# Performance work log

Measured on AMD Instinct MI355X. Metric: run time of the kernel, lower is better.

## Reference

```python
import jax, jax.numpy as jnp
import numpy as np
from jax import lax

B, N, IN_DIM, OUT_DIM = 4, 8192, 32, 128
NPOINT, RADIUS, NSAMPLE = 1024, 0.2, 32
BN_EPS = 1e-5

def _sqdist(a, b):
    # a: [B,n,3], b: [B,m,3] -> [B,n,m] squared euclidean distances
    return (jnp.sum(a * a, -1)[:, :, None] + jnp.sum(b * b, -1)[:, None, :]
            - 2.0 * jnp.einsum('bnd,bmd->bnm', a, b))

def _fps(xyz, npoint):
    # farthest point sampling, sequential by nature -> lax.scan over npoint steps
    Bn, Np, _ = xyz.shape
    def step(carry, _):
        dist, far = carry
        centroid = jnp.take_along_axis(xyz, far[:, None, None], axis=1)  # [B,1,3]
        dist = jnp.minimum(dist, jnp.sum((xyz - centroid) ** 2, -1))
        return (dist, jnp.argmax(dist, -1).astype(jnp.int32)), far
    init = (jnp.full((Bn, Np), 1e10, xyz.dtype), jnp.zeros((Bn,), jnp.int32))
    _, idx = lax.scan(step, init, None, length=npoint)
    return idx.T  # [B, npoint]

def _gather_points(x, idx):  # x [B,N,D], idx [B,...] -> [B,...,D]
    return jax.vmap(lambda p, i: p[i])(x, idx)

def _gather_feats(f, idx):  # f [B,C,N], idx [B,...] -> [B,C,...]
    return jax.vmap(lambda p, i: p[:, i])(f, idx)

def _ball_query(new_xyz, xyz):
    d2 = _sqdist(new_xyz, xyz)  # [B,P,N]
    Np = xyz.shape[1]
    cand = jnp.where(d2 < RADIUS ** 2, jnp.arange(Np, dtype=jnp.int32), Np)
    idx = -lax.top_k(-cand, NSAMPLE)[0]  # first NSAMPLE in-radius indices (sorted)
    return jnp.where(idx == Np, idx[..., :1], idx)  # pad misses with first hit

def _bn(x, gamma, beta, axes):
    # training-mode batch norm over `axes`, channel axis = 1
    m = jnp.mean(x, axes, keepdims=True)
    v = jnp.var(x, axes, keepdims=True)
    sh = (1, -1) + (1,) * (x.ndim - 2)
    return (x - m) * (gamma.reshape(sh) / jnp.sqrt(v + BN_EPS)) + beta.reshape(sh)

def _forward(xyz, features, W_sa0, g_sa0, b_sa0, W_sa1, g_sa1, b_sa1, W_sa2, g_sa2, b_sa2,
             W_fp0, g_fp0, b_fp0, W_fp1, g_fp1, b_fp1,
             Wc1, bc1, g1, b1, Wc2, bc2, g2, b2, Wc3, bc3):
    # --- PointnetSAModuleVotes: FPS + ball query + group (use_xyz, normalize_xyz) + MLP + maxpool ---
    fps_idx = _fps(xyz, NPOINT)
    new_xyz = _gather_points(xyz, fps_idx)                           # [B,P,3]
    gidx = _ball_query(new_xyz, xyz)                                 # [B,P,S]
    gxyz = (_gather_points(xyz, gidx) - new_xyz[:, :, None, :]) / RADIUS  # centered, normalized
    h = jnp.concatenate([gxyz.transpose(0, 3, 1, 2), _gather_feats(features, gidx)], 1)  # [B,3+C,P,S]
    for W, g, b in ((W_sa0, g_sa0, b_sa0), (W_sa1, g_sa1, b_sa1), (W_sa2, g_sa2, b_sa2)):
        h = jax.nn.relu(_bn(jnp.einsum('oc,bcps->bops', W, h), g, b, (0, 2, 3)))
    feat_sa = jnp.max(h, -1)                                         # [B,128,P]
    # --- PointnetFPModule: 3-NN interpolation (inv-sq-dist weights) + skip concat + MLP ---
    d2 = _sqdist(xyz, new_xyz)                                       # [B,N,P]
    neg, idx3 = lax.top_k(-d2, 3)
    recip = 1.0 / (jnp.maximum(-neg, 0.0) + 1e-8)
    w = recip / jnp.sum(recip, -1, keepdims=True)                    # [B,N,3]
    interp = jnp.sum(_gather_feats(feat_sa, idx3) * w[:, None, :, :], -1)  # [B,128,N]
    h = jnp.concatenate([interp, features], 1)                       # [B,128+C,N]
    for W, g, b in ((W_fp0, g_fp0, b_fp0), (W_fp1, g_fp1, b_fp1)):
        h = jax.nn.relu(_bn(jnp.einsum('oc,bcn->bon', W, h), g, b, (0, 2)))
    seed_features = h                                                # [B,128,N]
    # --- vote head: conv1d(1) + BN + ReLU x2, then conv1d(1) -> [3 offset | 1 score | out_dim feat] ---
    net = jax.nn.relu(_bn(jnp.einsum('oc,bcn->bon', Wc1, seed_features) + bc1[:, None], g1, b1, (0, 2)))
    net = jax.nn.relu(_bn(jnp.einsum('oc,bcn->bon', Wc2, net) + bc2[:, None], g2, b2, (0, 2)))
    net = (jnp.einsum('oc,bcn->bon', Wc3, net) + bc3[:, None]).transpose(0, 2, 1)  # [B,N,4+out]
    offset = net[:, :, 0:3]
    vote_xyz = xyz + offset
    vote_scores = jax.nn.sigmoid(net[:, :, 3])
    vf = seed_features.transpose(0, 2, 1) + net[:, :, 4:]
    vote_features = vf / jnp.maximum(jnp.linalg.norm(vf, axis=2, keepdims=True), 1e-12)  # F.normalize
    return vote_xyz, offset, vote_scores, vote_features

def setup_inputs():
    key = jax.random.key(0)
    ks = jax.random.split(key, 40)
    he = lambda k, o, c: jax.random.normal(k, (o, c), jnp.float32) * float(np.sqrt(2.0 / c))
    inp = {'xyz': jax.random.uniform(ks[0], (B, N, 3), jnp.float32),
           'features': jax.random.normal(ks[1], (B, IN_DIM, N), jnp.float32)}
    j = 2
    dims_sa = [IN_DIM + 3, 128, 128, 128]  # use_xyz adds 3 to first layer
    for i in range(3):
        inp[f'W_sa{i}'] = he(ks[j], 128, dims_sa[i]); j += 1
        inp[f'g_sa{i}'] = 1.0 + 0.1 * jax.random.normal(ks[j], (128,), jnp.float32); j += 1
        inp[f'b_sa{i}'] = 0.1 * jax.random.normal(ks[j], (128,), jnp.float32); j += 1
    dims_fp = [IN_DIM + 128, 128, 128]
    for i in range(2):
        inp[f'W_fp{i}'] = he(ks[j], 128, dims_fp[i]); j += 1
        inp[f'g_fp{i}'] = 1.0 + 0.1 * jax.random.normal(ks[j], (128,), jnp.float32); j += 1
        inp[f'b_fp{i}'] = 0.1 * jax.random.normal(ks[j], (128,), jnp.float32); j += 1
    inp['Wc1'] = he(ks[j], 128, 128); j += 1
    inp['bc1'] = 0.01 * jax.random.normal(ks[j], (128,), jnp.float32); j += 1
    inp['g1'] = 1.0 + 0.1 * jax.random.normal(ks[j], (128,), jnp.float32); j += 1
    inp['b1'] = 0.1 * jax.random.normal(ks[j], (128,), jnp.float32); j += 1
    inp['Wc2'] = he(ks[j], 128, 128); j += 1
    inp['bc2'] = 0.01 * jax.random.normal(ks[j], (128,), jnp.float32); j += 1
    inp['g2'] = 1.0 + 0.1 * jax.random.normal(ks[j], (128,), jnp.float32); j += 1
    inp['b2'] = 0.1 * jax.random.normal(ks[j], (128,), jnp.float32); j += 1
    inp['Wc3'] = he(ks[j], 4 + OUT_DIM, 128); j += 1
    inp['bc3'] = 0.01 * jax.random.normal(ks[j], (4 + OUT_DIM,), jnp.float32); j += 1
    return inp

def reference(xyz, features, W_sa0, g_sa0, b_sa0, W_sa1, g_sa1, b_sa1, W_sa2, g_sa2, b_sa2,
              W_fp0, g_fp0, b_fp0, W_fp1, g_fp1, b_fp1,
              Wc1, bc1, g1, b1, Wc2, bc2, g2, b2, Wc3, bc3):
    return _forward(xyz, features, W_sa0, g_sa0, b_sa0, W_sa1, g_sa1, b_sa1, W_sa2, g_sa2, b_sa2,
                    W_fp0, g_fp0, b_fp0, W_fp1, g_fp1, b_fp1,
                    Wc1, bc1, g1, b1, Wc2, bc2, g2, b2, Wc3, bc3)
```

## Files before the change

kernel.cpp:

```cpp
#include <hip/hip_runtime.h>
#include <hip/hip_bf16.h>
#include <math.h>

namespace {

constexpr int BB  = 4;
constexpr int NN  = 8192;
constexpr int IND = 32;
constexpr int NPT = 1024;
constexpr int NSM = 32;
constexpr int SACOLS = BB * NPT * NSM;
constexpr int FPCOLS = BB * NN;
constexpr int CSTR = 132;

__device__ __forceinline__ double sqn3_f64(float x, float y, float z) {
#pragma clang fp contract(off)
    double dx = (double)x, dy = (double)y, dz = (double)z;
    return (dx * dx + dy * dy) + dz * dz;
}
__device__ __forceinline__ double dot3_f64(float ax, float ay, float az,
                                           float bx, float by, float bz) {
#pragma clang fp contract(off)
    return ((double)ax * (double)bx + (double)ay * (double)by) + (double)az * (double)bz;
}
__device__ __forceinline__ double sqd_f64(double sa, double sb, double dot) {
#pragma clang fp contract(off)
    return (sa + sb) - 2.0 * dot;
}

__global__ __launch_bounds__(512)
void k_fps(const float* __restrict__ xyz, float* __restrict__ new_xyz)
{
#pragma clang fp contract(off)
    const int b   = blockIdx.x;
    const int tid = threadIdx.x;
    const float* P = xyz + (size_t)b * NN * 3;

    __shared__ float sx[NN];
    __shared__ float sy[NN];
    __shared__ float sz[NN];
    __shared__ float ctrs[NPT * 3];
    __shared__ unsigned long long wv[2][8];

    float px[16], py[16], pz[16], dd[16];
#pragma unroll
    for (int i = 0; i < 16; ++i) {
        int p = tid + i * 512;
        float x = P[p * 3 + 0], y = P[p * 3 + 1], z = P[p * 3 + 2];
        px[i] = x; py[i] = y; pz[i] = z; dd[i] = 1e10f;
        sx[p] = x; sy[p] = y; sz[p] = z;
    }
    float cx = P[0], cy = P[1], cz = P[2];
    __syncthreads();

    for (int t = 0; t < NPT; ++t) {
        if (tid == 0) {
            ctrs[t * 3 + 0] = cx;
            ctrs[t * 3 + 1] = cy;
            ctrs[t * 3 + 2] = cz;
        }
        if (t == NPT - 1) break;

        unsigned long long best = 0ull;
#pragma unroll
        for (int i = 0; i < 16; ++i) {
            float dx = px[i] - cx;
            float dy = py[i] - cy;
            float dz = pz[i] - cz;
            float d  = (dx * dx + dy * dy) + dz * dz;
            float nd = fminf(dd[i], d);
            dd[i] = nd;
            unsigned int lo = (unsigned)(NN - 1) - (unsigned)(tid + i * 512);
            unsigned long long cand =
                ((unsigned long long)__float_as_uint(nd) << 32) | lo;
            best = (cand > best) ? cand : best;
        }
        for (int off = 32; off > 0; off >>= 1) {
            unsigned long long o = __shfl_down(best, off);
            best = (o > best) ? o : best;
        }
        const int buf = t & 1;
        if ((tid & 63) == 0) wv[buf][tid >> 6] = best;
        __syncthreads();
        unsigned long long w0 = wv[buf][0];
#pragma unroll
        for (int k = 1; k < 8; ++k) {
            unsigned long long wk = wv[buf][k];
            w0 = (wk > w0) ? wk : w0;
        }
        const int idx = (NN - 1) - (int)(unsigned)(w0 & 0xFFFFFFFFull);
        cx = sx[idx]; cy = sy[idx]; cz = sz[idx];
    }

    __syncthreads();
    float* O = new_xyz + (size_t)b * NPT * 3;
    for (int i = tid; i < NPT * 3; i += 512) O[i] = ctrs[i];
}

__global__ __launch_bounds__(256)
void k_ballquery(const float* __restrict__ xyz, const float* __restrict__ new_xyz,
                 int* __restrict__ gidx)
{
    const int wv   = threadIdx.x >> 6;
    const int lane = threadIdx.x & 63;
    const int cid  = blockIdx.x * 4 + wv;
    const int b    = cid >> 10;
    const float* P = xyz + (size_t)b * NN * 3;

    const float cx = new_xyz[(size_t)cid * 3 + 0];
    const float cy = new_xyz[(size_t)cid * 3 + 1];
    const float cz = new_xyz[(size_t)cid * 3 + 2];
    const double sa = sqn3_f64(cx, cy, cz);
    const double R2 = 0.2 * 0.2;

    int cnt = 0;
    int firstidx = -1;
    int* G = gidx + (size_t)cid * NSM;

    for (int base = 0; base < NN && cnt < NSM; base += 64) {
        int p = base + lane;
        float x = P[p * 3 + 0], y = P[p * 3 + 1], z = P[p * 3 + 2];
        double sb  = sqn3_f64(x, y, z);
        double dot = dot3_f64(cx, cy, cz, x, y, z);
        double d2  = sqd_f64(sa, sb, dot);
        bool hit = d2 < R2;
        unsigned long long m = __ballot(hit);
        if (firstidx < 0 && m != 0ull) firstidx = base + __builtin_ctzll(m);
        int before = __popcll(m & ((1ull << lane) - 1ull));
        int pos = cnt + before;
        if (hit && pos < NSM) G[pos] = p;
        cnt += __popcll(m);
    }
    if (firstidx < 0) firstidx = 0;
    if (cnt < NSM) {
        for (int j = cnt + lane; j < NSM; j += 64) G[j] = firstidx;
    }
}

__global__ __launch_bounds__(256)
void k_group(const float* __restrict__ xyz, const float* __restrict__ feats,
             const float* __restrict__ new_xyz, const int* __restrict__ gidx,
             float* __restrict__ h0)
{
    const int col = blockIdx.x * 256 + threadIdx.x;
    const int cid = col >> 5;
    const int b   = col >> 15;
    const int g   = gidx[col];
    const float* Pt = xyz + ((size_t)b * NN + g) * 3;
    const float* Ct = new_xyz + (size_t)cid * 3;
    h0[(size_t)0 * SACOLS + col] = __fsub_rn(Pt[0], Ct[0]) / 0.2f;
    h0[(size_t)1 * SACOLS + col] = __fsub_rn(Pt[1], Ct[1]) / 0.2f;
    h0[(size_t)2 * SACOLS + col] = __fsub_rn(Pt[2], Ct[2]) / 0.2f;
    const float* FT = feats + (size_t)b * IND * NN;
    for (int c = 0; c < IND; ++c)
        h0[(size_t)(3 + c) * SACOLS + col] = FT[(size_t)c * NN + g];
}

__global__ __launch_bounds__(256)
void k_conv(const float* __restrict__ X, const float* __restrict__ W,
            const float* __restrict__ bias,
            const float* __restrict__ scale, const float* __restrict__ shift,
            float* __restrict__ Z, int Cin, int Cout, int ncol, int apply_act)
{
    __shared__ __align__(16) float Xs[32][64];
    __shared__ float Ws[64][33];
    const int tid  = threadIdx.x;
    const int col0 = blockIdx.x * 64;
    const int o0   = blockIdx.y * 64;
    const int tx   = tid & 15;
    const int ty   = tid >> 4;
    float acc[4][4] = {};

    for (int kk = 0; kk < Cin; kk += 32) {
#pragma unroll
        for (int i = 0; i < 8; ++i) {
            int idx = tid + i * 256;
            int c = idx >> 6, cc = idx & 63;
            int ch = kk + c;
            float v = 0.0f;
            if (ch < Cin) {
                v = X[(size_t)ch * ncol + col0 + cc];
                if (apply_act) v = fmaxf(fmaf(v, scale[ch], shift[ch]), 0.0f);
            }
            Xs[c][cc] = v;
        }
#pragma unroll
        for (int i = 0; i < 8; ++i) {
            int idx = tid + i * 256;
            int o = idx >> 5, c = idx & 31;
            int ch = kk + c, oo = o0 + o;
            Ws[o][c] = (ch < Cin && oo < Cout) ? W[(size_t)oo * Cin + ch] : 0.0f;
        }
        __syncthreads();
#pragma unroll
        for (int c = 0; c < 32; ++c) {
            const float4 xv = *reinterpret_cast<const float4*>(&Xs[c][tx * 4]);
            float w0 = Ws[ty * 4 + 0][c];
            float w1 = Ws[ty * 4 + 1][c];
            float w2 = Ws[ty * 4 + 2][c];
            float w3 = Ws[ty * 4 + 3][c];
            acc[0][0] = fmaf(w0, xv.x, acc[0][0]); acc[0][1] = fmaf(w0, xv.y, acc[0][1]);
            acc[0][2] = fmaf(w0, xv.z, acc[0][2]); acc[0][3] = fmaf(w0, xv.w, acc[0][3]);
            acc[1][0] = fmaf(w1, xv.x, acc[1][0]); acc[1][1] = fmaf(w1, xv.y, acc[1][1]);
            acc[1][2] = fmaf(w1, xv.z, acc[1][2]); acc[1][3] = fmaf(w1, xv.w, acc[1][3]);
            acc[2][0] = fmaf(w2, xv.x, acc[2][0]); acc[2][1] = fmaf(w2, xv.y, acc[2][1]);
            acc[2][2] = fmaf(w2, xv.z, acc[2][2]); acc[2][3] = fmaf(w2, xv.w, acc[2][3]);
            acc[3][0] = fmaf(w3, xv.x, acc[3][0]); acc[3][1] = fmaf(w3, xv.y, acc[3][1]);
            acc[3][2] = fmaf(w3, xv.z, acc[3][2]); acc[3][3] = fmaf(w3, xv.w, acc[3][3]);
        }
        __syncthreads();
    }
#pragma unroll
    for (int i = 0; i < 4; ++i) {
        int o = o0 + ty * 4 + i;
        if (o >= Cout) break;
        float bz = bias ? bias[o] : 0.0f;
#pragma unroll
        for (int j = 0; j < 4; ++j)
            Z[(size_t)o * ncol + col0 + tx * 4 + j] = acc[i][j] + bz;
    }
}

__global__ __launch_bounds__(256)
void k_stats_partial(const float* __restrict__ Z, double* __restrict__ part, int ncol, int nb)
{
    const int c = blockIdx.x, blk = blockIdx.y;
    const int chunk = ncol / nb;
    const float* p = Z + (size_t)c * ncol + (size_t)blk * chunk;
    double s = 0.0, q = 0.0;
    for (int j = threadIdx.x; j < chunk; j += 256) { double v = (double)p[j]; s += v; q += v * v; }
    __shared__ double ss[256];
    __shared__ double qq[256];
    ss[threadIdx.x] = s; qq[threadIdx.x] = q;
    __syncthreads();
    for (int off = 128; off > 0; off >>= 1) {
        if (threadIdx.x < off) { ss[threadIdx.x] += ss[threadIdx.x + off]; qq[threadIdx.x] += qq[threadIdx.x + off]; }
        __syncthreads();
    }
    if (threadIdx.x == 0) {
        part[(size_t)(c * nb + blk) * 2 + 0] = ss[0];
        part[(size_t)(c * nb + blk) * 2 + 1] = qq[0];
    }
}

__global__ void k_stats_final(const double* __restrict__ part,
                              const float* __restrict__ gamma, const float* __restrict__ beta,
                              float* __restrict__ sc_out, float* __restrict__ sh_out,
                              int C, int nb, double n)
{
    int c = threadIdx.x;
    if (c >= C) return;
    double s = 0.0, q = 0.0;
    for (int i = 0; i < nb; ++i) {
        s += part[(size_t)(c * nb + i) * 2 + 0];
        q += part[(size_t)(c * nb + i) * 2 + 1];
    }
    double mean = s / n;
    double var  = q / n - mean * mean;
    double scl  = (double)gamma[c] / sqrt(var + 1e-5);
    sc_out[c] = (float)scl;
    sh_out[c] = (float)((double)beta[c] - mean * scl);
}

__global__ __launch_bounds__(256)
void k_maxpool(const float* __restrict__ Z, const float* __restrict__ sc,
               const float* __restrict__ sh, float* __restrict__ feat)
{
    const int idx = blockIdx.x * 256 + threadIdx.x;
    const int bp  = idx & 4095;
    const int c   = idx >> 12;
    const float s = sc[c], h = sh[c];
    const float* p = Z + (size_t)c * SACOLS + (size_t)bp * 32;
    float m = 0.0f;
    for (int ss = 0; ss < 32; ++ss) m = fmaxf(m, fmaxf(fmaf(p[ss], s, h), 0.0f));
    feat[(size_t)c * (BB * NPT) + bp] = m;
}

__global__ __launch_bounds__(256)
void k_3nn(const float* __restrict__ xyz, const float* __restrict__ new_xyz,
           int* __restrict__ idx3, float* __restrict__ w3)
{
    const int gid = blockIdx.x * 256 + threadIdx.x;
    const int b = gid >> 13;
    __shared__ float  cxs[NPT];
    __shared__ float  cys[NPT];
    __shared__ float  czs[NPT];
    __shared__ double cns[NPT];
    const float* C = new_xyz + (size_t)b * NPT * 3;
    for (int i = threadIdx.x; i < NPT; i += 256) {
        float x = C[i * 3], y = C[i * 3 + 1], z = C[i * 3 + 2];
        cxs[i] = x; cys[i] = y; czs[i] = z; cns[i] = sqn3_f64(x, y, z);
    }
    __syncthreads();

    const float* P = xyz + (size_t)gid * 3;
    const float px = P[0], py = P[1], pz = P[2];
    const double sb = sqn3_f64(px, py, pz);
    double d0 = 1e30, d1 = 1e30, d2v = 1e30;
    int    i0 = 0, i1 = 0, i2 = 0;
    for (int m = 0; m < NPT; ++m) {
        double dot = dot3_f64(px, py, pz, cxs[m], cys[m], czs[m]);
        double d   = sqd_f64(sb, cns[m], dot);
        if (d < d0)       { d2v = d1; i2 = i1; d1 = d0; i1 = i0; d0 = d; i0 = m; }
        else if (d < d1)  { d2v = d1; i2 = i1; d1 = d;  i1 = m; }
        else if (d < d2v) { d2v = d;  i2 = m; }
    }
    {
#pragma clang fp contract(off)
        double e0 = fmax(d0, 0.0), e1 = fmax(d1, 0.0), e2 = fmax(d2v, 0.0);
        double r0 = 1.0 / (e0 + 1e-8);
        double r1 = 1.0 / (e1 + 1e-8);
        double r2 = 1.0 / (e2 + 1e-8);
        double rs = (r0 + r1) + r2;
        idx3[(size_t)gid * 3 + 0] = i0; idx3[(size_t)gid * 3 + 1] = i1; idx3[(size_t)gid * 3 + 2] = i2;
        w3[(size_t)gid * 3 + 0] = (float)(r0 / rs);
        w3[(size_t)gid * 3 + 1] = (float)(r1 / rs);
        w3[(size_t)gid * 3 + 2] = (float)(r2 / rs);
    }
}

__global__ __launch_bounds__(256)
void k_hfp(const float* __restrict__ feats, const float* __restrict__ feat_sa,
           const int* __restrict__ idx3, const float* __restrict__ w3,
           float* __restrict__ hfp)
{
    const int col = blockIdx.x * 256 + threadIdx.x;
    const int b = col >> 13, n = col & 8191;
    const int ia = idx3[(size_t)col * 3 + 0];
    const int ib = idx3[(size_t)col * 3 + 1];
    const int ic = idx3[(size_t)col * 3 + 2];
    const float wa = w3[(size_t)col * 3 + 0];
    const float wb = w3[(size_t)col * 3 + 1];
    const float wc = w3[(size_t)col * 3 + 2];
    const int cb = b * NPT;
    for (int o = 0; o < 128; ++o) {
        const float* f = feat_sa + (size_t)o * (BB * NPT) + cb;
        hfp[(size_t)o * FPCOLS + col] = f[ia] * wa + f[ib] * wb + f[ic] * wc;
    }
    const float* FT = feats + (size_t)b * IND * NN;
    for (int c = 0; c < IND; ++c)
        hfp[(size_t)(128 + c) * FPCOLS + col] = FT[(size_t)c * NN + n];
}

__global__ __launch_bounds__(256)
void k_outputs(const float* __restrict__ xyz, const float* __restrict__ Zc3,
               const float* __restrict__ Zf1, const float* __restrict__ sc4,
               const float* __restrict__ sh4, float* __restrict__ out)
{
    const int col = blockIdx.x * 256 + threadIdx.x;
    const float n0 = Zc3[(size_t)0 * FPCOLS + col];
    const float n1 = Zc3[(size_t)1 * FPCOLS + col];
    const float n2 = Zc3[(size_t)2 * FPCOLS + col];
    const float n3 = Zc3[(size_t)3 * FPCOLS + col];
    const float* P = xyz + (size_t)col * 3;

    float* o_vxyz = out;
    float* o_off  = out + 98304;
    float* o_sc   = out + 196608;
    float* o_vf   = out + 229376;

    o_off[(size_t)col * 3 + 0] = n0;
    o_off[(size_t)col * 3 + 1] = n1;
    o_off[(size_t)col * 3 + 2] = n2;
    o_vxyz[(size_t)col * 3 + 0] = __fadd_rn(P[0], n0);
    o_vxyz[(size_t)col * 3 + 1] = __fadd_rn(P[1], n1);
    o_vxyz[(size_t)col * 3 + 2] = __fadd_rn(P[2], n2);
    o_sc[col] = 1.0f / (1.0f + expf(-n3));

    float sumsq = 0.0f;
    for (int c = 0; c < 128; ++c) {
        float seed = fmaxf(fmaf(Zf1[(size_t)c * FPCOLS + col], sc4[c], sh4[c]), 0.0f);
        float v = seed + Zc3[(size_t)(4 + c) * FPCOLS + col];
        sumsq = fmaf(v, v, sumsq);
    }
    float inv = 1.0f / fmaxf(sqrtf(sumsq), 1e-12f);
    for (int c = 0; c < 128; ++c) {
        float seed = fmaxf(fmaf(Zf1[(size_t)c * FPCOLS + col], sc4[c], sh4[c]), 0.0f);
        float v = seed + Zc3[(size_t)(4 + c) * FPCOLS + col];
        o_vf[(size_t)col * 128 + c] = v * inv;
    }
}

__global__ void k_sentinel(float* out)
{
    if (threadIdx.x < 8) out[threadIdx.x] = 12345.0f;
}

}

extern "C" void kernel_launch(void* const* d_in, const int* in_sizes, int n_in,
                              void* d_out, int out_size, void* d_ws, size_t ws_size,
                              hipStream_t stream)
{
    (void)in_sizes; (void)n_in; (void)out_size;
    const float* xyz   = (const float*)d_in[0];
    const float* feats = (const float*)d_in[1];
    const float* W_sa0 = (const float*)d_in[2];
    const float* g_sa0 = (const float*)d_in[3];
    const float* b_sa0 = (const float*)d_in[4];
    const float* W_sa1 = (const float*)d_in[5];
    const float* g_sa1 = (const float*)d_in[6];
    const float* b_sa1 = (const float*)d_in[7];
    const float* W_sa2 = (const float*)d_in[8];
    const float* g_sa2 = (const float*)d_in[9];
    const float* b_sa2 = (const float*)d_in[10];
    const float* W_fp0 = (const float*)d_in[11];
    const float* g_fp0 = (const float*)d_in[12];
    const float* b_fp0 = (const float*)d_in[13];
    const float* W_fp1 = (const float*)d_in[14];
    const float* g_fp1 = (const float*)d_in[15];
    const float* b_fp1 = (const float*)d_in[16];
    const float* Wc1   = (const float*)d_in[17];
    const float* bc1   = (const float*)d_in[18];
    const float* g1    = (const float*)d_in[19];
    const float* b1    = (const float*)d_in[20];
    const float* Wc2   = (const float*)d_in[21];
    const float* bc2   = (const float*)d_in[22];
    const float* g2    = (const float*)d_in[23];
    const float* b2    = (const float*)d_in[24];
    const float* Wc3   = (const float*)d_in[25];
    const float* bc3   = (const float*)d_in[26];

    char* ws = (char*)d_ws;
    size_t off = 0;
    auto alloc = [&](size_t bytes) -> size_t {
        size_t o = off;
        off += (bytes + 255) & ~(size_t)255;
        return o;
    };
    float*  new_xyz = (float*) (ws + alloc((size_t)BB * NPT * 3 * 4));
    int*    gidx    = (int*)   (ws + alloc((size_t)BB * NPT * NSM * 4));
    int*    idx3    = (int*)   (ws + alloc((size_t)FPCOLS * 3 * 4));
    float*  w3      = (float*) (ws + alloc((size_t)FPCOLS * 3 * 4));
    double* part    = (double*)(ws + alloc((size_t)132 * 32 * 2 * 8));
    float*  stats   = (float*) (ws + alloc((size_t)7 * 2 * CSTR * 4));
    float*  regA    = (float*) (ws + alloc((size_t)35 * SACOLS * 4));
    float*  ZA      = (float*) (ws + alloc((size_t)128 * SACOLS * 4));
    float*  ZB      = (float*) (ws + alloc((size_t)128 * SACOLS * 4));
    float*  feat_sa = (float*) (ws + alloc((size_t)128 * BB * NPT * 4));
    size_t required = off;

    if (ws_size < required) {
        k_sentinel<<<1, 64, 0, stream>>>((float*)d_out);
        return;
    }

    float* h0  = regA;
    float* Zc3 = regA;
    float* hfp = ZA;
    float* Zf0 = ZA + (size_t)160 * FPCOLS;
    float* Zc1 = ZA + (size_t)(160 + 128) * FPCOLS;
    float* Zf1 = ZB;
    float* Zc2 = ZB + (size_t)128 * FPCOLS;

    float* st[7];
    for (int l = 0; l < 7; ++l) st[l] = stats + (size_t)l * 2 * CSTR;
    const double nSA = (double)SACOLS, nFP = (double)FPCOLS;

    k_fps<<<BB, 512, 0, stream>>>(xyz, new_xyz);
    k_ballquery<<<(BB * NPT) / 4, 256, 0, stream>>>(xyz, new_xyz, gidx);
    k_group<<<SACOLS / 256, 256, 0, stream>>>(xyz, feats, new_xyz, gidx, h0);

    k_conv<<<dim3(SACOLS / 64, 2), 256, 0, stream>>>(h0, W_sa0, nullptr, nullptr, nullptr, ZA, 35, 128, SACOLS, 0);
    k_stats_partial<<<dim3(128, 32), 256, 0, stream>>>(ZA, part, SACOLS, 32);
    k_stats_final<<<1, 256, 0, stream>>>(part, g_sa0, b_sa0, st[0], st[0] + CSTR, 128, 32, nSA);

    k_conv<<<dim3(SACOLS / 64, 2), 256, 0, stream>>>(ZA, W_sa1, nullptr, st[0], st[0] + CSTR, ZB, 128, 128, SACOLS, 1);
    k_stats_partial<<<dim3(128, 32), 256, 0, stream>>>(ZB, part, SACOLS, 32);
    k_stats_final<<<1, 256, 0, stream>>>(part, g_sa1, b_sa1, st[1], st[1] + CSTR, 128, 32, nSA);

    k_conv<<<dim3(SACOLS / 64, 2), 256, 0, stream>>>(ZB, W_sa2, nullptr, st[1], st[1] + CSTR, ZA, 128, 128, SACOLS, 1);
    k_stats_partial<<<dim3(128, 32), 256, 0, stream>>>(ZA, part, SACOLS, 32);
    k_stats_final<<<1, 256, 0, stream>>>(part, g_sa2, b_sa2, st[2], st[2] + CSTR, 128, 32, nSA);

    k_maxpool<<<(128 * BB * NPT) / 256, 256, 0, stream>>>(ZA, st[2], st[2] + CSTR, feat_sa);

    k_3nn<<<FPCOLS / 256, 256, 0, stream>>>(xyz, new_xyz, idx3, w3);
    k_hfp<<<FPCOLS / 256, 256, 0, stream>>>(feats, feat_sa, idx3, w3, hfp);

    k_conv<<<dim3(FPCOLS / 64, 2), 256, 0, stream>>>(hfp, W_fp0, nullptr, nullptr, nullptr, Zf0, 160, 128, FPCOLS, 0);
    k_stats_partial<<<dim3(128, 32), 256, 0, stream>>>(Zf0, part, FPCOLS, 32);
    k_stats_final<<<1, 256, 0, stream>>>(part, g_fp0, b_fp0, st[3], st[3] + CSTR, 128, 32, nFP);

    k_conv<<<dim3(FPCOLS / 64, 2), 256, 0, stream>>>(Zf0, W_fp1, nullptr, st[3], st[3] + CSTR, Zf1, 128, 128, FPCOLS, 1);
    k_stats_partial<<<dim3(128, 32), 256, 0, stream>>>(Zf1, part, FPCOLS, 32);
    k_stats_final<<<1, 256, 0, stream>>>(part, g_fp1, b_fp1, st[4], st[4] + CSTR, 128, 32, nFP);

    k_conv<<<dim3(FPCOLS / 64, 2), 256, 0, stream>>>(Zf1, Wc1, bc1, st[4], st[4] + CSTR, Zc1, 128, 128, FPCOLS, 1);
    k_stats_partial<<<dim3(128, 32), 256, 0, stream>>>(Zc1, part, FPCOLS, 32);
    k_stats_final<<<1, 256, 0, stream>>>(part, g1, b1, st[5], st[5] + CSTR, 128, 32, nFP);

    k_conv<<<dim3(FPCOLS / 64, 2), 256, 0, stream>>>(Zc1, Wc2, bc2, st[5], st[5] + CSTR, Zc2, 128, 128, FPCOLS, 1);
    k_stats_partial<<<dim3(128, 32), 256, 0, stream>>>(Zc2, part, FPCOLS, 32);
    k_stats_final<<<1, 256, 0, stream>>>(part, g2, b2, st[6], st[6] + CSTR, 128, 32, nFP);

    k_conv<<<dim3(FPCOLS / 64, 3), 256, 0, stream>>>(Zc2, Wc3, bc3, st[6], st[6] + CSTR, Zc3, 128, 132, FPCOLS, 1);

    k_outputs<<<FPCOLS / 256, 256, 0, stream>>>(xyz, Zc3, Zf1, st[4], st[4] + CSTR, (float*)d_out);
}
```

Baseline: 2.426 ms.

## Enlarge conv register tile to 8x4 and halve FPS block size

The conv GEMM kernel now computes a 64x128 output tile per block, with each thread holding 8x4 accumulators. Weights are stored transposed in shared memory so each thread reads them as two float4 loads, which raises arithmetic intensity per shared-memory load. Separately, FPS drops to 256 threads per block with 32 points per thread, so the per-step reduction involves fewer wavefronts. The trade-offs are higher register pressure in conv, fewer conv blocks in flight, and more serial work per FPS thread.

After: 2.518 ms. +3.8%, slower.

```diff
diff --git a/kernel.cpp b/kernel.cpp
--- a/kernel.cpp
+++ b/kernel.cpp
@@ -28,7 +28,7 @@
     return (sa + sb) - 2.0 * dot;
 }
 
-__global__ __launch_bounds__(512)
+__global__ __launch_bounds__(256)
 void k_fps(const float* __restrict__ xyz, float* __restrict__ new_xyz)
 {
 #pragma clang fp contract(off)
@@ -40,12 +40,12 @@
     __shared__ float sy[NN];
     __shared__ float sz[NN];
     __shared__ float ctrs[NPT * 3];
-    __shared__ unsigned long long wv[2][8];
-
-    float px[16], py[16], pz[16], dd[16];
-#pragma unroll
-    for (int i = 0; i < 16; ++i) {
-        int p = tid + i * 512;
+    __shared__ unsigned long long wv[2][4];
+
+    float px[32], py[32], pz[32], dd[32];
+#pragma unroll
+    for (int i = 0; i < 32; ++i) {
+        int p = tid + i * 256;
         float x = P[p * 3 + 0], y = P[p * 3 + 1], z = P[p * 3 + 2];
         px[i] = x; py[i] = y; pz[i] = z; dd[i] = 1e10f;
         sx[p] = x; sy[p] = y; sz[p] = z;
@@ -63,14 +63,14 @@
 
         unsigned long long best = 0ull;
 #pragma unroll
-        for (int i = 0; i < 16; ++i) {
+        for (int i = 0; i < 32; ++i) {
             float dx = px[i] - cx;
             float dy = py[i] - cy;
             float dz = pz[i] - cz;
             float d  = (dx * dx + dy * dy) + dz * dz;
             float nd = fminf(dd[i], d);
             dd[i] = nd;
-            unsigned int lo = (unsigned)(NN - 1) - (unsigned)(tid + i * 512);
+            unsigned int lo = (unsigned)(NN - 1) - (unsigned)(tid + i * 256);
             unsigned long long cand =
                 ((unsigned long long)__float_as_uint(nd) << 32) | lo;
             best = (cand > best) ? cand : best;
@@ -84,7 +84,7 @@
         __syncthreads();
         unsigned long long w0 = wv[buf][0];
 #pragma unroll
-        for (int k = 1; k < 8; ++k) {
+        for (int k = 1; k < 4; ++k) {
             unsigned long long wk = wv[buf][k];
             w0 = (wk > w0) ? wk : w0;
         }
@@ -94,7 +94,7 @@
 
     __syncthreads();
     float* O = new_xyz + (size_t)b * NPT * 3;
-    for (int i = tid; i < NPT * 3; i += 512) O[i] = ctrs[i];
+    for (int i = tid; i < NPT * 3; i += 256) O[i] = ctrs[i];
 }
 
 __global__ __launch_bounds__(256)
@@ -162,20 +162,20 @@
             const float* __restrict__ scale, const float* __restrict__ shift,
             float* __restrict__ Z, int Cin, int Cout, int ncol, int apply_act)
 {
-    __shared__ __align__(16) float Xs[32][64];
-    __shared__ float Ws[64][33];
+    __shared__ __align__(16) float Xs[32][128];
+    __shared__ __align__(16) float Ws[32][72];
     const int tid  = threadIdx.x;
-    const int col0 = blockIdx.x * 64;
+    const int col0 = blockIdx.x * 128;
     const int o0   = blockIdx.y * 64;
-    const int tx   = tid & 15;
-    const int ty   = tid >> 4;
-    float acc[4][4] = {};
+    const int tx   = tid & 31;
+    const int ty   = tid >> 5;
+    float acc[8][4] = {};
 
     for (int kk = 0; kk < Cin; kk += 32) {
 #pragma unroll
-        for (int i = 0; i < 8; ++i) {
+        for (int i = 0; i < 16; ++i) {
             int idx = tid + i * 256;
-            int c = idx >> 6, cc = idx & 63;
+            int c = idx >> 7, cc = idx & 127;
             int ch = kk + c;
             float v = 0.0f;
             if (ch < Cin) {
@@ -189,35 +189,43 @@
             int idx = tid + i * 256;
             int o = idx >> 5, c = idx & 31;
             int ch = kk + c, oo = o0 + o;
-            Ws[o][c] = (ch < Cin && oo < Cout) ? W[(size_t)oo * Cin + ch] : 0.0f;
+            Ws[c][o] = (ch < Cin && oo < Cout) ? W[(size_t)oo * Cin + ch] : 0.0f;
         }
         __syncthreads();
 #pragma unroll
         for (int c = 0; c < 32; ++c) {
             const float4 xv = *reinterpret_cast<const float4*>(&Xs[c][tx * 4]);
-            float w0 = Ws[ty * 4 + 0][c];
-            float w1 = Ws[ty * 4 + 1][c];
-            float w2 = Ws[ty * 4 + 2][c];
-            float w3 = Ws[ty * 4 + 3][c];
-            acc[0][0] = fmaf(w0, xv.x, acc[0][0]); acc[0][1] = fmaf(w0, xv.y, acc[0][1]);
-            acc[0][2] = fmaf(w0, xv.z, acc[0][2]); acc[0][3] = fmaf(w0, xv.w, acc[0][3]);
-            acc[1][0] = fmaf(w1, xv.x, acc[1][0]); acc[1][1] = fmaf(w1, xv.y, acc[1][1]);
-            acc[1][2] = fmaf(w1, xv.z, acc[1][2]); acc[1][3] = fmaf(w1, xv.w, acc[1][3]);
-            acc[2][0] = fmaf(w2, xv.x, acc[2][0]); acc[2][1] = fmaf(w2, xv.y, acc[2][1]);
-            acc[2][2] = fmaf(w2, xv.z, acc[2][2]); acc[2][3] = fmaf(w2, xv.w, acc[2][3]);
-            acc[3][0] = fmaf(w3, xv.x, acc[3][0]); acc[3][1] = fmaf(w3, xv.y, acc[3][1]);
-            acc[3][2] = fmaf(w3, xv.z, acc[3][2]); acc[3][3] = fmaf(w3, xv.w, acc[3][3]);
+            const float4 wa = *reinterpret_cast<const float4*>(&Ws[c][ty * 8]);
+            const float4 wb = *reinterpret_cast<const float4*>(&Ws[c][ty * 8 + 4]);
+            acc[0][0] = fmaf(wa.x, xv.x, acc[0][0]); acc[0][1] = fmaf(wa.x, xv.y, acc[0][1]);
+            acc[0][2] = fmaf(wa.x, xv.z, acc[0][2]); acc[0][3] = fmaf(wa.x, xv.w, acc[0][3]);
+            acc[1][0] = fmaf(wa.y, xv.x, acc[1][0]); acc[1][1] = fmaf(wa.y, xv.y, acc[1][1]);
+            acc[1][2] = fmaf(wa.y, xv.z, acc[1][2]); acc[1][3] = fmaf(wa.y, xv.w, acc[1][3]);
+            acc[2][0] = fmaf(wa.z, xv.x, acc[2][0]); acc[2][1] = fmaf(wa.z, xv.y, acc[2][1]);
+            acc[2][2] = fmaf(wa.z, xv.z, acc[2][2]); acc[2][3] = fmaf(wa.z, xv.w, acc[2][3]);
+            acc[3][0] = fmaf(wa.w, xv.x, acc[3][0]); acc[3][1] = fmaf(wa.w, xv.y, acc[3][1]);
+            acc[3][2] = fmaf(wa.w, xv.z, acc[3][2]); acc[3][3] = fmaf(wa.w, xv.w, acc[3][3]);
+            acc[4][0] = fmaf(wb.x, xv.x, acc[4][0]); acc[4][1] = fmaf(wb.x, xv.y, acc[4][1]);
+            acc[4][2] = fmaf(wb.x, xv.z, acc[4][2]); acc[4][3] = fmaf(wb.x, xv.w, acc[4][3]);
+            acc[5][0] = fmaf(wb.y, xv.x, acc[5][0]); acc[5][1] = fmaf(wb.y, xv.y, acc[5][1]);
+            acc[5][2] = fmaf(wb.y, xv.z, acc[5][2]); acc[5][3] = fmaf(wb.y, xv.w, acc[5][3]);
+            acc[6][0] = fmaf(wb.z, xv.x, acc[6][0]); acc[6][1] = fmaf(wb.z, xv.y, acc[6][1]);
+            acc[6][2] = fmaf(wb.z, xv.z, acc[6][2]); acc[6][3] = fmaf(wb.z, xv.w, acc[6][3]);
+            acc[7][0] = fmaf(wb.w, xv.x, acc[7][0]); acc[7][1] = fmaf(wb.w, xv.y, acc[7][1]);
+            acc[7][2] = fmaf(wb.w, xv.z, acc[7][2]); acc[7][3] = fmaf(wb.w, xv.w, acc[7][3]);
         }
         __syncthreads();
     }
 #pragma unroll
-    for (int i = 0; i < 4; ++i) {
-        int o = o0 + ty * 4 + i;
+    for (int j = 0; j < 8; ++j) {
+        int o = o0 + ty * 8 + j;
         if (o >= Cout) break;
         float bz = bias ? bias[o] : 0.0f;
-#pragma unroll
-        for (int j = 0; j < 4; ++j)
-            Z[(size_t)o * ncol + col0 + tx * 4 + j] = acc[i][j] + bz;
+        float* zp = Z + (size_t)o * ncol + col0 + tx * 4;
+        zp[0] = acc[j][0] + bz;
+        zp[1] = acc[j][1] + bz;
+        zp[2] = acc[j][2] + bz;
+        zp[3] = acc[j][3] + bz;
     }
 }
 
@@ -457,19 +465,19 @@
     for (int l = 0; l < 7; ++l) st[l] = stats + (size_t)l * 2 * CSTR;
     const double nSA = (double)SACOLS, nFP = (double)FPCOLS;
 
-    k_fps<<<BB, 512, 0, stream>>>(xyz, new_xyz);
+    k_fps<<<BB, 256, 0, stream>>>(xyz, new_xyz);
     k_ballquery<<<(BB * NPT) / 4, 256, 0, stream>>>(xyz, new_xyz, gidx);
     k_group<<<SACOLS / 256, 256, 0, stream>>>(xyz, feats, new_xyz, gidx, h0);
 
-    k_conv<<<dim3(SACOLS / 64, 2), 256, 0, stream>>>(h0, W_sa0, nullptr, nullptr, nullptr, ZA, 35, 128, SACOLS, 0);
+    k_conv<<<dim3(SACOLS / 128, 2), 256, 0, stream>>>(h0, W_sa0, nullptr, nullptr, nullptr, ZA, 35, 128, SACOLS, 0);
     k_stats_partial<<<dim3(128, 32), 256, 0, stream>>>(ZA, part, SACOLS, 32);
     k_stats_final<<<1, 256, 0, stream>>>(part, g_sa0, b_sa0, st[0], st[0] + CSTR, 128, 32, nSA);
 
-    k_conv<<<dim3(SACOLS / 64, 2), 256, 0, stream>>>(ZA, W_sa1, nullptr, st[0], st[0] + CSTR, ZB, 128, 128, SACOLS, 1);
+    k_conv<<<dim3(SACOLS / 128, 2), 256, 0, stream>>>(ZA, W_sa1, nullptr, st[0], st[0] + CSTR, ZB, 128, 128, SACOLS, 1);
     k_stats_partial<<<dim3(128, 32), 256, 0, stream>>>(ZB, part, SACOLS, 32);
     k_stats_final<<<1, 256, 0, stream>>>(part, g_sa1, b_sa1, st[1], st[1] + CSTR, 128, 32, nSA);
 
-    k_conv<<<dim3(SACOLS / 64, 2), 256, 0, stream>>>(ZB, W_sa2, nullptr, st[1], st[1] + CSTR, ZA, 128, 128, SACOLS, 1);
+    k_conv<<<dim3(SACOLS / 128, 2), 256, 0, stream>>>(ZB, W_sa2, nullptr, st[1], st[1] + CSTR, ZA, 128, 128, SACOLS, 1);
     k_stats_partial<<<dim3(128, 32), 256, 0, stream>>>(ZA, part, SACOLS, 32);
     k_stats_final<<<1, 256, 0, stream>>>(part, g_sa2, b_sa2, st[2], st[2] + CSTR, 128, 32, nSA);
 
@@ -478,23 +486,23 @@
     k_3nn<<<FPCOLS / 256, 256, 0, stream>>>(xyz, new_xyz, idx3, w3);
     k_hfp<<<FPCOLS / 256, 256, 0, stream>>>(feats, feat_sa, idx3, w3, hfp);
 
-    k_conv<<<dim3(FPCOLS / 64, 2), 256, 0, stream>>>(hfp, W_fp0, nullptr, nullptr, nullptr, Zf0, 160, 128, FPCOLS, 0);
+    k_conv<<<dim3(FPCOLS / 128, 2), 256, 0, stream>>>(hfp, W_fp0, nullptr, nullptr, nullptr, Zf0, 160, 128, FPCOLS, 0);
     k_stats_partial<<<dim3(128, 32), 256, 0, stream>>>(Zf0, part, FPCOLS, 32);
     k_stats_final<<<1, 256, 0, stream>>>(part, g_fp0, b_fp0, st[3], st[3] + CSTR, 128, 32, nFP);
 
-    k_conv<<<dim3(FPCOLS / 64, 2), 256, 0, stream>>>(Zf0, W_fp1, nullptr, st[3], st[3] + CSTR, Zf1, 128, 128, FPCOLS, 1);
+    k_conv<<<dim3(FPCOLS / 128, 2), 256, 0, stream>>>(Zf0, W_fp1, nullptr, st[3], st[3] + CSTR, Zf1, 128, 128, FPCOLS, 1);
     k_stats_partial<<<dim3(128, 32), 256, 0, stream>>>(Zf1, part, FPCOLS, 32);
     k_stats_final<<<1, 256, 0, stream>>>(part, g_fp1, b_fp1, st[4], st[4] + CSTR, 128, 32, nFP);
 
-    k_conv<<<dim3(FPCOLS / 64, 2), 256, 0, stream>>>(Zf1, Wc1, bc1, st[4], st[4] + CSTR, Zc1, 128, 128, FPCOLS, 1);
+    k_conv<<<dim3(FPCOLS / 128, 2), 256, 0, stream>>>(Zf1, Wc1, bc1, st[4], st[4] + CSTR, Zc1, 128, 128, FPCOLS, 1);
     k_stats_partial<<<dim3(128, 32), 256, 0, stream>>>(Zc1, part, FPCOLS, 32);
     k_stats_final<<<1, 256, 0, stream>>>(part, g1, b1, st[5], st[5] + CSTR, 128, 32, nFP);
 
-    k_conv<<<dim3(FPCOLS / 64, 2), 256, 0, stream>>>(Zc1, Wc2, bc2, st[5], st[5] + CSTR, Zc2, 128, 128, FPCOLS, 1);
+    k_conv<<<dim3(FPCOLS / 128, 2), 256, 0, stream>>>(Zc1, Wc2, bc2, st[5], st[5] + CSTR, Zc2, 128, 128, FPCOLS, 1);
     k_stats_partial<<<dim3(128, 32), 256, 0, stream>>>(Zc2, part, FPCOLS, 32);
     k_stats_final<<<1, 256, 0, stream>>>(part, g2, b2, st[6], st[6] + CSTR, 128, 32, nFP);
 
-    k_conv<<<dim3(FPCOLS / 64, 3), 256, 0, stream>>>(Zc2, Wc3, bc3, st[6], st[6] + CSTR, Zc3, 128, 132, FPCOLS, 1);
+    k_conv<<<dim3(FPCOLS / 128, 3), 256, 0, stream>>>(Zc2, Wc3, bc3, st[6], st[6] + CSTR, Zc3, 128, 132, FPCOLS, 1);
 
     k_outputs<<<FPCOLS / 256, 256, 0, stream>>>(xyz, Zc3, Zf1, st[4], st[4] + CSTR, (float*)d_out);
 }
```
